# Kernel tuning notes

Measured on AMD Instinct MI355X. Metric: run time of the kernel, lower is better.

Reference implementation:

```python
import jax, jax.numpy as jnp
import numpy as np

N = 100000   # nodes
E = 1600000  # edges
D_IN, D_H, D_OUT = 128, 128, 64
BN_EPS = 1e-5


def setup_inputs() -> dict:
    key = jax.random.key(0)
    ks = jax.random.split(key, 12)

    def lin_w(k, fan_in, shape):
        s = 1.0 / np.sqrt(fan_in)
        return jax.random.uniform(k, shape, jnp.float32, -s, s)

    return {
        "x": jax.random.normal(ks[0], (N, D_IN), jnp.float32),
        "edge_index": jax.random.randint(ks[1], (2, E), 0, N, dtype=jnp.int64),
        "edge_weight": jax.random.uniform(ks[2], (E,), jnp.float32),
        "W1": lin_w(ks[3], D_IN, (D_IN, D_H)),
        "b1": jnp.zeros((D_H,), jnp.float32),
        "W2": lin_w(ks[4], D_H, (D_H, D_H)),
        "b2": jnp.zeros((D_H,), jnp.float32),
        "W3": lin_w(ks[5], D_H, (D_H, D_OUT)),
        "b3": jnp.zeros((D_OUT,), jnp.float32),
        "gamma1": jnp.ones((D_H,), jnp.float32),
        "beta1": jnp.zeros((D_H,), jnp.float32),
        "gamma2": jnp.ones((D_H,), jnp.float32),
        "beta2": jnp.zeros((D_H,), jnp.float32),
    }


def _gcn_conv(x, src, dst, w, W, b):
    # PyG GCNConv: x' = D^{-1/2} (A + I) D^{-1/2} (x W) + b, self-loop weight 1
    n = x.shape[0]
    h = x @ W                                   # [N, d_out]
    loop = jnp.arange(n, dtype=src.dtype)
    s = jnp.concatenate([src, loop])            # [E+N]
    d = jnp.concatenate([dst, loop])
    ww = jnp.concatenate([w, jnp.ones((n,), w.dtype)])
    deg = jax.ops.segment_sum(ww, d, num_segments=n)          # in-degree at targets
    dinv = jnp.where(deg > 0, jax.lax.rsqrt(deg), 0.0)
    norm = dinv[s] * ww * dinv[d]               # [E+N]
    msg = h[s] * norm[:, None]                  # gather + scale
    out = jax.ops.segment_sum(msg, d, num_segments=n)
    return out + b


def _batch_norm(x, gamma, beta):
    mean = jnp.mean(x, axis=0)
    var = jnp.mean(jnp.square(x - mean), axis=0)  # biased, as BatchNorm uses
    return (x - mean) * jax.lax.rsqrt(var + BN_EPS) * gamma + beta


def reference(x, edge_index, edge_weight, W1, b1, W2, b2, W3, b3,
              gamma1, beta1, gamma2, beta2):
    src, dst = edge_index[0], edge_index[1]
    h = _gcn_conv(x, src, dst, edge_weight, W1, b1)
    h = jax.nn.relu(_batch_norm(h, gamma1, beta1))
    h = _gcn_conv(h, src, dst, edge_weight, W2, b2)
    h = jax.nn.relu(_batch_norm(h, gamma2, beta2))
    return _gcn_conv(h, src, dst, edge_weight, W3, b3)
```

## Files before the change

### kernel.cpp

```cpp
#include <hip/hip_runtime.h>
#include <hip/hip_fp16.h>
#include <cstdint>
#include <cstddef>

#define BN_EPS 1e-5f
#define FPSCALE 268435456.0f

typedef _Float16 half8 __attribute__((ext_vector_type(8)));
typedef float floatx4 __attribute__((ext_vector_type(4)));

__device__ __forceinline__ float loadS(const __half* p) { return __half2float(*p); }
__device__ __forceinline__ float2 load2(const __half* p) {
    return __half22float2(*(const __half2*)p);
}
__device__ __forceinline__ void storeS(float* p, float v) { *p = v; }
__device__ __forceinline__ void storeS(__half* p, float v) { *p = __float2half(v); }
__device__ __forceinline__ void store2(float* p, float a, float b) {
    *(float2*)p = make_float2(a, b);
}
__device__ __forceinline__ void store2(__half* p, float a, float b) {
    *(__half2*)p = __floats2half2_rn(a, b);
}
__device__ __forceinline__ float wn_of(unsigned v) {
    __half_raw hr; hr.x = (unsigned short)(v & 0x7fffu);
    return __half2float((__half)hr);
}

__global__ void detect_mode_kernel(const unsigned* __restrict__ p, int nwords, int* mode) {
    __shared__ unsigned red[256];
    unsigned m = 0;
    for (int i = 1 + 2 * (int)threadIdx.x; i < nwords; i += 512) m |= p[i];
    red[threadIdx.x] = m;
    __syncthreads();
    for (int s = 128; s > 0; s >>= 1) {
        if ((int)threadIdx.x < s) red[threadIdx.x] |= red[threadIdx.x + s];
        __syncthreads();
    }
    if (threadIdx.x == 0) mode[0] = (red[0] == 0) ? 1 : 0;
}

static __device__ __forceinline__ int load_edge(const void* ei, int mode64, long long pos) {
    if (mode64) return (int)((const long long*)ei)[pos];
    return ((const int*)ei)[pos];
}

__global__ void fill_packed_kernel(unsigned long long* __restrict__ packed, int N) {
    int i = blockIdx.x * 256 + threadIdx.x;
    if (i < N) packed[i] = 0ULL;
}

__global__ void histogram_kernel(const void* __restrict__ ei, const float* __restrict__ ew,
                                 unsigned long long* __restrict__ packed,
                                 unsigned* __restrict__ rank,
                                 const int* __restrict__ mode, int E) {
    int e = blockIdx.x * 256 + threadIdx.x;
    if (e >= E) return;
    int md = *mode;
    int d = load_edge(ei, md, (long long)E + e);
    unsigned long long contrib = (1ULL << 40) | (unsigned long long)(ew[e] * FPSCALE);
    unsigned long long old = atomicAdd(&packed[d], contrib);
    rank[e] = (unsigned)(old >> 40);
}

__global__ void unpack_kernel(const unsigned long long* __restrict__ packed,
                              float* __restrict__ dinv, int* __restrict__ cnt, int N) {
    int i = blockIdx.x * 256 + threadIdx.x;
    if (i < N) {
        unsigned long long p = packed[i];
        cnt[i] = (int)(p >> 40);
        float deg = 1.0f + (float)(p & 0xFFFFFFFFFFULL) * (1.0f / FPSCALE);
        dinv[i] = rsqrtf(deg);
    }
}

__global__ void scan_phaseA_kernel(const int* __restrict__ cnt, int* __restrict__ bsum, int N) {
    __shared__ int red[256];
    int base = blockIdx.x * 2048 + (int)threadIdx.x * 8;
    int s = 0;
#pragma unroll
    for (int j = 0; j < 8; ++j) { int idx = base + j; if (idx < N) s += cnt[idx]; }
    red[threadIdx.x] = s;
    __syncthreads();
    for (int st = 128; st > 0; st >>= 1) {
        if ((int)threadIdx.x < st) red[threadIdx.x] += red[threadIdx.x + st];
        __syncthreads();
    }
    if (threadIdx.x == 0) bsum[blockIdx.x] = red[0];
}

__global__ void scan_phaseB_kernel(int* __restrict__ bsum, int G) {
    if (threadIdx.x == 0 && blockIdx.x == 0) {
        int run = 0;
        for (int i = 0; i < G; ++i) { int t = bsum[i]; bsum[i] = run; run += t; }
    }
}

__global__ void scan_phaseC_kernel(const int* __restrict__ cnt, const int* __restrict__ bsum,
                                   int* __restrict__ row_start, int N) {
    __shared__ int lds[256];
    int tid = threadIdx.x;
    int base = blockIdx.x * 2048 + tid * 8;
    int vals[8];
    int s = 0;
#pragma unroll
    for (int j = 0; j < 8; ++j) {
        int idx = base + j;
        int v = (idx < N) ? cnt[idx] : 0;
        vals[j] = s;
        s += v;
    }
    lds[tid] = s;
    __syncthreads();
    for (int off = 1; off < 256; off <<= 1) {
        int t = 0;
        if (tid >= off) t = lds[tid - off];
        __syncthreads();
        lds[tid] += t;
        __syncthreads();
    }
    int excl = lds[tid] - s;
    int b = bsum[blockIdx.x] + excl;
#pragma unroll
    for (int j = 0; j < 8; ++j) {
        int idx = base + j;
        if (idx < N) row_start[idx] = b + vals[j];
    }
}

__global__ void scatter_kernel(const void* __restrict__ ei, const float* __restrict__ ew,
                               const float* __restrict__ dinv,
                               const int* __restrict__ row_start,
                               const unsigned* __restrict__ rank,
                               unsigned* __restrict__ edata,
                               const int* __restrict__ mode, int E) {
    int e = blockIdx.x * 256 + threadIdx.x;
    if (e >= E) return;
    int md = *mode;
    int s = load_edge(ei, md, e);
    int d = load_edge(ei, md, (long long)E + e);
    float wn = dinv[s] * ew[e] * dinv[d];
    unsigned hb = (unsigned)__half_as_ushort(__float2half(wn)) & 0x7fffu;
    edata[row_start[d] + (int)rank[e]] = ((unsigned)s << 15) | hb;
}

template <int M>
__global__ void transpose_w_kernel(const float* __restrict__ W, _Float16* __restrict__ WT) {
    int t = blockIdx.x * 256 + (int)threadIdx.x;
    if (t < 128 * M) {
        int n = t / 128, k = t % 128;
        WT[t] = (_Float16)W[k * M + n];
    }
}

template <int M, bool BN, typename TI>
__global__ __launch_bounds__(256) void gemm_mfma_kernel(const TI* __restrict__ X,
                                                        const _Float16* __restrict__ WTg,
                                                        const float* __restrict__ sc,
                                                        const float* __restrict__ sh,
                                                        __half* __restrict__ Hout, int N) {
    constexpr int CT = M / 16;
    constexpr int LDK = 128 + 8;
    __shared__ _Float16 WT[M * LDK];

    for (int t = threadIdx.x; t < M * 16; t += 256) {
        int n = t / 16, seg = t % 16;
        *(half8*)&WT[n * LDK + seg * 8] = *(const half8*)&WTg[n * 128 + seg * 8];
    }
    __syncthreads();

    const int wave = (int)threadIdx.x >> 6;
    const int lane = (int)threadIdx.x & 63;
    const int qd = lane >> 4;
    const int ln = lane & 15;
    const int tile0 = blockIdx.x * 64 + wave * 16;
    int ar = tile0 + ln;
    if (ar >= N) ar = N - 1;

    half8 aF[4];
    const TI* xr = X + (size_t)ar * 128 + qd * 8;
#pragma unroll
    for (int kb = 0; kb < 4; ++kb) {
        float vv[8];
        if constexpr (sizeof(TI) == 4) {
            float4 v0 = *(const float4*)(xr + kb * 32);
            float4 v1 = *(const float4*)(xr + kb * 32 + 4);
            vv[0] = v0.x; vv[1] = v0.y; vv[2] = v0.z; vv[3] = v0.w;
            vv[4] = v1.x; vv[5] = v1.y; vv[6] = v1.z; vv[7] = v1.w;
        } else {
            half8 raw = *(const half8*)(xr + kb * 32);
#pragma unroll
            for (int j = 0; j < 8; ++j) vv[j] = (float)raw[j];
        }
        if (BN) {
            const int kbase = kb * 32 + qd * 8;
#pragma unroll
            for (int j = 0; j < 8; ++j)
                vv[j] = fmaxf(fmaf(vv[j], sc[kbase + j], sh[kbase + j]), 0.0f);
        }
        half8 a;
#pragma unroll
        for (int j = 0; j < 8; ++j) a[j] = (_Float16)vv[j];
        aF[kb] = a;
    }

#pragma unroll
    for (int ct = 0; ct < CT; ++ct) {
        floatx4 acc = {0.0f, 0.0f, 0.0f, 0.0f};
#pragma unroll
        for (int kb = 0; kb < 4; ++kb) {
            half8 b = *(const half8*)&WT[(ct * 16 + ln) * LDK + kb * 32 + qd * 8];
            acc = __builtin_amdgcn_mfma_f32_16x16x32_f16(aF[kb], b, acc, 0, 0, 0);
        }
#pragma unroll
        for (int r = 0; r < 4; ++r) {
            int orow = tile0 + qd * 4 + r;
            if (orow < N) Hout[(size_t)orow * M + ct * 16 + ln] = __float2half(acc[r]);
        }
    }
}

template <int D, bool BIAS, typename TY>
__global__ __launch_bounds__(64) void agg_kernel(const __half* __restrict__ H,
                                                 const unsigned* __restrict__ edata,
                                                 const int* __restrict__ row_start,
                                                 const int* __restrict__ cnt,
                                                 const float* __restrict__ dinv,
                                                 const float* __restrict__ bias,
                                                 TY* __restrict__ Y, int N) {
    constexpr int VPT = D / 64;
    __shared__ unsigned eb[64];
    const int i = blockIdx.x;
    const int t = (int)threadIdx.x;
    const int c0 = t * VPT;
    const float di = dinv[i];
    const float dii = di * di;

    float acc0, acc1 = 0.0f;
    if constexpr (VPT == 2) {
        float2 h = load2(H + (size_t)i * D + c0);
        acc0 = dii * h.x;
        acc1 = dii * h.y;
    } else {
        acc0 = dii * loadS(H + (size_t)i * D + c0);
    }

    const int base = row_start[i];
    const int n = cnt[i];
    for (int off = 0; off < n; off += 64) {
        const int m = min(64, n - off);
        if (t < m) eb[t] = edata[base + off + t];
        __syncthreads();
        int j = 0;
        for (; j + 4 <= m; j += 4) {
            const unsigned e0 = eb[j], e1 = eb[j + 1], e2 = eb[j + 2], e3 = eb[j + 3];
            const float w0 = wn_of(e0), w1 = wn_of(e1), w2 = wn_of(e2), w3 = wn_of(e3);
            if constexpr (VPT == 2) {
                float2 h0 = load2(H + (size_t)(e0 >> 15) * D + c0);
                float2 h1 = load2(H + (size_t)(e1 >> 15) * D + c0);
                float2 h2 = load2(H + (size_t)(e2 >> 15) * D + c0);
                float2 h3 = load2(H + (size_t)(e3 >> 15) * D + c0);
                acc0 = fmaf(w0, h0.x, acc0); acc1 = fmaf(w0, h0.y, acc1);
                acc0 = fmaf(w1, h1.x, acc0); acc1 = fmaf(w1, h1.y, acc1);
                acc0 = fmaf(w2, h2.x, acc0); acc1 = fmaf(w2, h2.y, acc1);
                acc0 = fmaf(w3, h3.x, acc0); acc1 = fmaf(w3, h3.y, acc1);
            } else {
                float h0 = loadS(H + (size_t)(e0 >> 15) * D + c0);
                float h1 = loadS(H + (size_t)(e1 >> 15) * D + c0);
                float h2 = loadS(H + (size_t)(e2 >> 15) * D + c0);
                float h3 = loadS(H + (size_t)(e3 >> 15) * D + c0);
                acc0 = fmaf(w0, h0, acc0);
                acc0 = fmaf(w1, h1, acc0);
                acc0 = fmaf(w2, h2, acc0);
                acc0 = fmaf(w3, h3, acc0);
            }
        }
        for (; j < m; ++j) {
            const unsigned e = eb[j];
            const float wn = wn_of(e);
            const size_t rb = (size_t)(e >> 15) * D + c0;
            if constexpr (VPT == 2) {
                float2 h = load2(H + rb);
                acc0 = fmaf(wn, h.x, acc0);
                acc1 = fmaf(wn, h.y, acc1);
            } else {
                acc0 = fmaf(wn, loadS(H + rb), acc0);
            }
        }
        __syncthreads();
    }

    if constexpr (VPT == 2) {
        if (BIAS) { acc0 += bias[c0]; acc1 += bias[c0 + 1]; }
        store2(Y + (size_t)i * D + c0, acc0, acc1);
    } else {
        if (BIAS) acc0 += bias[c0];
        storeS(Y + (size_t)i * D + c0, acc0);
    }
}

__global__ void zero_stats_kernel(float* __restrict__ gsum, float* __restrict__ gsq) {
    int t = threadIdx.x;
    if (t < 128) { gsum[t] = 0.0f; gsq[t] = 0.0f; }
}

__global__ void stats_kernel(const __half* __restrict__ Y, float* __restrict__ gsum,
                             float* __restrict__ gsq, int N) {
    __shared__ float ls[256], lq[256];
    const int tid = threadIdx.x;
    const int c = tid & 127;
    const int half_ = tid >> 7;
    float s = 0.0f, q = 0.0f;
    for (int row = blockIdx.x * 2 + half_; row < N; row += 512) {
        float v = __half2float(Y[(size_t)row * 128 + c]);
        s += v;
        q = fmaf(v, v, q);
    }
    ls[tid] = s; lq[tid] = q;
    __syncthreads();
    if (tid < 128) {
        atomicAdd(&gsum[c], ls[tid] + ls[tid + 128]);
        atomicAdd(&gsq[c],  lq[tid] + lq[tid + 128]);
    }
}

__global__ void finalize_stats_kernel(const float* __restrict__ gsum, const float* __restrict__ gsq,
                                      const float* __restrict__ gamma, const float* __restrict__ beta,
                                      float* __restrict__ sc, float* __restrict__ sh, int N) {
    int t = threadIdx.x;
    if (t < 128) {
        float inv_n = 1.0f / (float)N;
        float mean = gsum[t] * inv_n;
        float var = gsq[t] * inv_n - mean * mean;
        float scale = gamma[t] * rsqrtf(var + BN_EPS);
        sc[t] = scale;
        sh[t] = beta[t] - mean * scale;
    }
}

extern "C" void kernel_launch(void* const* d_in, const int* in_sizes, int n_in,
                              void* d_out, int out_size, void* d_ws, size_t ws_size,
                              hipStream_t stream) {
    const float* x   = (const float*)d_in[0];
    const void*  ei  = d_in[1];
    const float* ew  = (const float*)d_in[2];
    const float* W1  = (const float*)d_in[3];
    const float* W2  = (const float*)d_in[5];
    const float* W3  = (const float*)d_in[7];
    const float* b3  = (const float*)d_in[8];
    const float* g1  = (const float*)d_in[9];
    const float* be1 = (const float*)d_in[10];
    const float* g2  = (const float*)d_in[11];
    const float* be2 = (const float*)d_in[12];
    float* out = (float*)d_out;

    const int N = in_sizes[0] / 128;
    const int E = in_sizes[2];
    const int G = (N + 2047) / 2048;

    char* w = (char*)d_ws;
    size_t off = 0;
    auto alloc = [&](size_t bytes) -> void* {
        void* p = w + off;
        off += (bytes + 255) & ~(size_t)255;
        return p;
    };
    unsigned long long* packed = (unsigned long long*)alloc((size_t)N * 8);
    float* dinv      = (float*)alloc((size_t)N * 4);
    int*   cnt       = (int*)  alloc((size_t)N * 4);
    int*   row_start = (int*)  alloc((size_t)N * 4);
    unsigned* rank   = (unsigned*)alloc((size_t)E * 4);
    unsigned* edata  = (unsigned*)alloc((size_t)E * 4);
    int*   bsum      = (int*)  alloc((size_t)G * 4);
    int*   mode      = (int*)  alloc(256);
    float* gsum      = (float*)alloc(128 * 4);
    float* gsq       = (float*)alloc(128 * 4);
    float* scb       = (float*)alloc(128 * 4);
    float* shb       = (float*)alloc(128 * 4);
    _Float16* WT1    = (_Float16*)alloc(128 * 128 * 2);
    _Float16* WT2    = (_Float16*)alloc(128 * 128 * 2);
    _Float16* WT3    = (_Float16*)alloc(128 * 64 * 2);
    __half* H        = (__half*)alloc((size_t)N * 128 * 2);
    __half* Yh       = (__half*)alloc((size_t)N * 128 * 2);
    (void)ws_size; (void)n_in; (void)out_size;

    const int nb = (N + 255) / 256;
    const int ebk = (E + 255) / 256;
    const int gb = (N + 63) / 64;

    detect_mode_kernel<<<1, 256, 0, stream>>>((const unsigned*)ei, 4096, mode);
    fill_packed_kernel<<<nb, 256, 0, stream>>>(packed, N);
    histogram_kernel<<<ebk, 256, 0, stream>>>(ei, ew, packed, rank, mode, E);
    unpack_kernel<<<nb, 256, 0, stream>>>(packed, dinv, cnt, N);
    scan_phaseA_kernel<<<G, 256, 0, stream>>>(cnt, bsum, N);
    scan_phaseB_kernel<<<1, 1, 0, stream>>>(bsum, G);
    scan_phaseC_kernel<<<G, 256, 0, stream>>>(cnt, bsum, row_start, N);
    scatter_kernel<<<ebk, 256, 0, stream>>>(ei, ew, dinv, row_start, rank, edata, mode, E);

    transpose_w_kernel<128><<<64, 256, 0, stream>>>(W1, WT1);
    transpose_w_kernel<128><<<64, 256, 0, stream>>>(W2, WT2);
    transpose_w_kernel<64><<<32, 256, 0, stream>>>(W3, WT3);

    gemm_mfma_kernel<128, false, float><<<gb, 256, 0, stream>>>(x, WT1, nullptr, nullptr, H, N);
    agg_kernel<128, false, __half><<<N, 64, 0, stream>>>(H, edata, row_start, cnt, dinv, nullptr, Yh, N);
    zero_stats_kernel<<<1, 128, 0, stream>>>(gsum, gsq);
    stats_kernel<<<256, 256, 0, stream>>>(Yh, gsum, gsq, N);
    finalize_stats_kernel<<<1, 128, 0, stream>>>(gsum, gsq, g1, be1, scb, shb, N);

    gemm_mfma_kernel<128, true, __half><<<gb, 256, 0, stream>>>(Yh, WT2, scb, shb, H, N);
    agg_kernel<128, false, __half><<<N, 64, 0, stream>>>(H, edata, row_start, cnt, dinv, nullptr, Yh, N);
    zero_stats_kernel<<<1, 128, 0, stream>>>(gsum, gsq);
    stats_kernel<<<256, 256, 0, stream>>>(Yh, gsum, gsq, N);
    finalize_stats_kernel<<<1, 128, 0, stream>>>(gsum, gsq, g2, be2, scb, shb, N);

    gemm_mfma_kernel<64, true, __half><<<gb, 256, 0, stream>>>(Yh, WT3, scb, shb, H, N);
    agg_kernel<64, true, float><<<N, 64, 0, stream>>>(H, edata, row_start, cnt, dinv, b3, out, N);
}
```

Before: 562.6 us.

## Merge setup kernels and run graph aggregation with shuffle broadcast, four nodes per block

Combines many small launches into fewer kernels. Mode detection, packed zeroing and weight transposes now share one init kernel. The histogram runs alongside the first GEMM. Unpack is merged with scan phase A, and the serial phase B is replaced by a per-block prefix sum in scan C. Stats zeroing is folded into the scatter and GEMM kernels. The aggregation kernel now handles four nodes per 256-thread block, one wave per node. It broadcasts edge data with wave shuffles instead of LDS and __syncthreads, and unrolls the gather loop by eight, relying on padded zero-weight entries for the tail. The aim is to cut launch overhead and barrier cost, in exchange for a little redundant bsum summation and extra gathers of row 0 on the tail.

```diff
diff --git a/kernel.cpp b/kernel.cpp
--- a/kernel.cpp
+++ b/kernel.cpp
@@ -26,141 +26,65 @@
     return __half2float((__half)hr);
 }
 
-__global__ void detect_mode_kernel(const unsigned* __restrict__ p, int nwords, int* mode) {
-    __shared__ unsigned red[256];
-    unsigned m = 0;
-    for (int i = 1 + 2 * (int)threadIdx.x; i < nwords; i += 512) m |= p[i];
-    red[threadIdx.x] = m;
-    __syncthreads();
-    for (int s = 128; s > 0; s >>= 1) {
-        if ((int)threadIdx.x < s) red[threadIdx.x] |= red[threadIdx.x + s];
-        __syncthreads();
-    }
-    if (threadIdx.x == 0) mode[0] = (red[0] == 0) ? 1 : 0;
-}
-
 static __device__ __forceinline__ int load_edge(const void* ei, int mode64, long long pos) {
     if (mode64) return (int)((const long long*)ei)[pos];
     return ((const int*)ei)[pos];
 }
 
-__global__ void fill_packed_kernel(unsigned long long* __restrict__ packed, int N) {
-    int i = blockIdx.x * 256 + threadIdx.x;
-    if (i < N) packed[i] = 0ULL;
-}
-
-__global__ void histogram_kernel(const void* __restrict__ ei, const float* __restrict__ ew,
-                                 unsigned long long* __restrict__ packed,
-                                 unsigned* __restrict__ rank,
-                                 const int* __restrict__ mode, int E) {
-    int e = blockIdx.x * 256 + threadIdx.x;
-    if (e >= E) return;
-    int md = *mode;
-    int d = load_edge(ei, md, (long long)E + e);
-    unsigned long long contrib = (1ULL << 40) | (unsigned long long)(ew[e] * FPSCALE);
-    unsigned long long old = atomicAdd(&packed[d], contrib);
-    rank[e] = (unsigned)(old >> 40);
-}
-
-__global__ void unpack_kernel(const unsigned long long* __restrict__ packed,
-                              float* __restrict__ dinv, int* __restrict__ cnt, int N) {
-    int i = blockIdx.x * 256 + threadIdx.x;
-    if (i < N) {
-        unsigned long long p = packed[i];
-        cnt[i] = (int)(p >> 40);
-        float deg = 1.0f + (float)(p & 0xFFFFFFFFFFULL) * (1.0f / FPSCALE);
-        dinv[i] = rsqrtf(deg);
-    }
-}
-
-__global__ void scan_phaseA_kernel(const int* __restrict__ cnt, int* __restrict__ bsum, int N) {
-    __shared__ int red[256];
-    int base = blockIdx.x * 2048 + (int)threadIdx.x * 8;
-    int s = 0;
-#pragma unroll
-    for (int j = 0; j < 8; ++j) { int idx = base + j; if (idx < N) s += cnt[idx]; }
-    red[threadIdx.x] = s;
-    __syncthreads();
-    for (int st = 128; st > 0; st >>= 1) {
-        if ((int)threadIdx.x < st) red[threadIdx.x] += red[threadIdx.x + st];
+__global__ __launch_bounds__(256) void init_kernel(const unsigned* __restrict__ eiw, int nwords,
+                                                   int* __restrict__ mode,
+                                                   unsigned long long* __restrict__ packed, int N,
+                                                   const float* __restrict__ W1,
+                                                   const float* __restrict__ W2,
+                                                   const float* __restrict__ W3,
+                                                   _Float16* __restrict__ WT1,
+                                                   _Float16* __restrict__ WT2,
+                                                   _Float16* __restrict__ WT3, int nb) {
+    __shared__ unsigned red[256];
+    const int bid = (int)blockIdx.x;
+    const int tid = (int)threadIdx.x;
+    if (bid < nb) {
+        int i = bid * 256 + tid;
+        if (i < N) packed[i] = 0ULL;
+        return;
+    }
+    if (bid == nb) {
+        unsigned m = 0;
+        for (int i = 1 + 2 * tid; i < nwords; i += 512) m |= eiw[i];
+        red[tid] = m;
         __syncthreads();
-    }
-    if (threadIdx.x == 0) bsum[blockIdx.x] = red[0];
-}
-
-__global__ void scan_phaseB_kernel(int* __restrict__ bsum, int G) {
-    if (threadIdx.x == 0 && blockIdx.x == 0) {
-        int run = 0;
-        for (int i = 0; i < G; ++i) { int t = bsum[i]; bsum[i] = run; run += t; }
-    }
-}
-
-__global__ void scan_phaseC_kernel(const int* __restrict__ cnt, const int* __restrict__ bsum,
-                                   int* __restrict__ row_start, int N) {
-    __shared__ int lds[256];
-    int tid = threadIdx.x;
-    int base = blockIdx.x * 2048 + tid * 8;
-    int vals[8];
-    int s = 0;
-#pragma unroll
-    for (int j = 0; j < 8; ++j) {
-        int idx = base + j;
-        int v = (idx < N) ? cnt[idx] : 0;
-        vals[j] = s;
-        s += v;
-    }
-    lds[tid] = s;
-    __syncthreads();
-    for (int off = 1; off < 256; off <<= 1) {
-        int t = 0;
-        if (tid >= off) t = lds[tid - off];
-        __syncthreads();
-        lds[tid] += t;
-        __syncthreads();
-    }
-    int excl = lds[tid] - s;
-    int b = bsum[blockIdx.x] + excl;
-#pragma unroll
-    for (int j = 0; j < 8; ++j) {
-        int idx = base + j;
-        if (idx < N) row_start[idx] = b + vals[j];
-    }
-}
-
-__global__ void scatter_kernel(const void* __restrict__ ei, const float* __restrict__ ew,
-                               const float* __restrict__ dinv,
-                               const int* __restrict__ row_start,
-                               const unsigned* __restrict__ rank,
-                               unsigned* __restrict__ edata,
-                               const int* __restrict__ mode, int E) {
-    int e = blockIdx.x * 256 + threadIdx.x;
-    if (e >= E) return;
-    int md = *mode;
-    int s = load_edge(ei, md, e);
-    int d = load_edge(ei, md, (long long)E + e);
-    float wn = dinv[s] * ew[e] * dinv[d];
-    unsigned hb = (unsigned)__half_as_ushort(__float2half(wn)) & 0x7fffu;
-    edata[row_start[d] + (int)rank[e]] = ((unsigned)s << 15) | hb;
-}
-
-template <int M>
-__global__ void transpose_w_kernel(const float* __restrict__ W, _Float16* __restrict__ WT) {
-    int t = blockIdx.x * 256 + (int)threadIdx.x;
-    if (t < 128 * M) {
+        for (int s = 128; s > 0; s >>= 1) {
+            if (tid < s) red[tid] |= red[tid + s];
+            __syncthreads();
+        }
+        if (tid == 0) mode[0] = (red[0] == 0) ? 1 : 0;
+        return;
+    }
+    const int t_ = bid - nb - 1;
+    if (t_ < 64) {
+        int t = t_ * 256 + tid;
         int n = t / 128, k = t % 128;
-        WT[t] = (_Float16)W[k * M + n];
+        WT1[t] = (_Float16)W1[k * 128 + n];
+    } else if (t_ < 128) {
+        int t = (t_ - 64) * 256 + tid;
+        int n = t / 128, k = t % 128;
+        WT2[t] = (_Float16)W2[k * 128 + n];
+    } else {
+        int t = (t_ - 128) * 256 + tid;
+        int n = t / 128, k = t % 128;
+        WT3[t] = (_Float16)W3[k * 64 + n];
     }
 }
 
 template <int M, bool BN, typename TI>
-__global__ __launch_bounds__(256) void gemm_mfma_kernel(const TI* __restrict__ X,
-                                                        const _Float16* __restrict__ WTg,
-                                                        const float* __restrict__ sc,
-                                                        const float* __restrict__ sh,
-                                                        __half* __restrict__ Hout, int N) {
+__device__ __forceinline__ void gemm_body(int gbid, const TI* __restrict__ X,
+                                          const _Float16* __restrict__ WTg,
+                                          const float* __restrict__ sc,
+                                          const float* __restrict__ sh,
+                                          __half* __restrict__ Hout, int N,
+                                          _Float16* WT ) {
     constexpr int CT = M / 16;
-    constexpr int LDK = 128 + 8;
-    __shared__ _Float16 WT[M * LDK];
+    constexpr int LDK = 136;
 
     for (int t = threadIdx.x; t < M * 16; t += 256) {
         int n = t / 16, seg = t % 16;
@@ -172,7 +96,7 @@
     const int lane = (int)threadIdx.x & 63;
     const int qd = lane >> 4;
     const int ln = lane & 15;
-    const int tile0 = blockIdx.x * 64 + wave * 16;
+    const int tile0 = gbid * 64 + wave * 16;
     int ar = tile0 + ln;
     if (ar >= N) ar = N - 1;
 
@@ -219,19 +143,127 @@
     }
 }
 
+__global__ __launch_bounds__(256) void hist_gemm1_kernel(const void* __restrict__ ei,
+                                                         const float* __restrict__ ew,
+                                                         unsigned long long* __restrict__ packed,
+                                                         unsigned* __restrict__ rank,
+                                                         const int* __restrict__ mode, int E, int GB,
+                                                         const float* __restrict__ X,
+                                                         const _Float16* __restrict__ WT1g,
+                                                         __half* __restrict__ Hout, int N) {
+    __shared__ _Float16 WT[128 * 136];
+    if ((int)blockIdx.x < GB) {
+        gemm_body<128, false, float>(blockIdx.x, X, WT1g, nullptr, nullptr, Hout, N, WT);
+        return;
+    }
+    int e = ((int)blockIdx.x - GB) * 256 + (int)threadIdx.x;
+    if (e >= E) return;
+    int md = *mode;
+    int d = load_edge(ei, md, (long long)E + e);
+    unsigned long long contrib = (1ULL << 40) | (unsigned long long)(ew[e] * FPSCALE);
+    unsigned long long old = atomicAdd(&packed[d], contrib);
+    rank[e] = (unsigned)(old >> 40);
+}
+
+__global__ __launch_bounds__(256) void unpack_scanA_kernel(const unsigned long long* __restrict__ packed,
+                                                           float* __restrict__ dinv,
+                                                           int* __restrict__ cnt,
+                                                           int* __restrict__ bsum, int N) {
+    __shared__ int red[256];
+    const int tid = (int)threadIdx.x;
+    const int base = (int)blockIdx.x * 2048 + tid * 8;
+    int s = 0;
+#pragma unroll
+    for (int j = 0; j < 8; ++j) {
+        int idx = base + j;
+        if (idx < N) {
+            unsigned long long p = packed[idx];
+            int c = (int)(p >> 40);
+            cnt[idx] = c;
+            dinv[idx] = rsqrtf(1.0f + (float)(p & 0xFFFFFFFFFFULL) * (1.0f / FPSCALE));
+            s += c;
+        }
+    }
+    red[tid] = s;
+    __syncthreads();
+    for (int st = 128; st > 0; st >>= 1) {
+        if (tid < st) red[tid] += red[tid + st];
+        __syncthreads();
+    }
+    if (tid == 0) bsum[blockIdx.x] = red[0];
+}
+
+__global__ __launch_bounds__(256) void scanC_kernel(const int* __restrict__ cnt,
+                                                    const int* __restrict__ bsum,
+                                                    int* __restrict__ row_start, int N) {
+    __shared__ int lds[256];
+    const int tid = (int)threadIdx.x;
+    int gbase = 0;
+    for (int j = 0; j < (int)blockIdx.x; ++j) gbase += bsum[j];
+    const int base = (int)blockIdx.x * 2048 + tid * 8;
+    int vals[8];
+    int s = 0;
+#pragma unroll
+    for (int j = 0; j < 8; ++j) {
+        int idx = base + j;
+        int v = (idx < N) ? cnt[idx] : 0;
+        vals[j] = s;
+        s += v;
+    }
+    lds[tid] = s;
+    __syncthreads();
+    for (int off = 1; off < 256; off <<= 1) {
+        int t = 0;
+        if (tid >= off) t = lds[tid - off];
+        __syncthreads();
+        lds[tid] += t;
+        __syncthreads();
+    }
+    int excl = lds[tid] - s;
+    int b = gbase + excl;
+#pragma unroll
+    for (int j = 0; j < 8; ++j) {
+        int idx = base + j;
+        if (idx < N) row_start[idx] = b + vals[j];
+    }
+}
+
+__global__ __launch_bounds__(256) void scatter_zero_kernel(const void* __restrict__ ei,
+                                                           const float* __restrict__ ew,
+                                                           const float* __restrict__ dinv,
+                                                           const int* __restrict__ row_start,
+                                                           const unsigned* __restrict__ rank,
+                                                           unsigned* __restrict__ edata,
+                                                           const int* __restrict__ mode, int E, int EBK,
+                                                           float* __restrict__ gsum,
+                                                           float* __restrict__ gsq) {
+    if ((int)blockIdx.x == EBK) {
+        if (threadIdx.x < 128) { gsum[threadIdx.x] = 0.0f; gsq[threadIdx.x] = 0.0f; }
+        return;
+    }
+    int e = (int)blockIdx.x * 256 + (int)threadIdx.x;
+    if (e >= E) return;
+    int md = *mode;
+    int s = load_edge(ei, md, e);
+    int d = load_edge(ei, md, (long long)E + e);
+    float wn = dinv[s] * ew[e] * dinv[d];
+    unsigned hb = (unsigned)__half_as_ushort(__float2half(wn)) & 0x7fffu;
+    edata[row_start[d] + (int)rank[e]] = ((unsigned)s << 15) | hb;
+}
+
 template <int D, bool BIAS, typename TY>
-__global__ __launch_bounds__(64) void agg_kernel(const __half* __restrict__ H,
-                                                 const unsigned* __restrict__ edata,
-                                                 const int* __restrict__ row_start,
-                                                 const int* __restrict__ cnt,
-                                                 const float* __restrict__ dinv,
-                                                 const float* __restrict__ bias,
-                                                 TY* __restrict__ Y, int N) {
+__global__ __launch_bounds__(256) void agg_kernel(const __half* __restrict__ H,
+                                                  const unsigned* __restrict__ edata,
+                                                  const int* __restrict__ row_start,
+                                                  const int* __restrict__ cnt,
+                                                  const float* __restrict__ dinv,
+                                                  const float* __restrict__ bias,
+                                                  TY* __restrict__ Y, int N) {
     constexpr int VPT = D / 64;
-    __shared__ unsigned eb[64];
-    const int i = blockIdx.x;
-    const int t = (int)threadIdx.x;
-    const int c0 = t * VPT;
+    const int lane = (int)threadIdx.x & 63;
+    const int i = (int)blockIdx.x * 4 + ((int)threadIdx.x >> 6);
+    if (i >= N) return;
+    const int c0 = lane * VPT;
     const float di = dinv[i];
     const float dii = di * di;
 
@@ -247,46 +279,51 @@
     const int base = row_start[i];
     const int n = cnt[i];
     for (int off = 0; off < n; off += 64) {
-        const int m = min(64, n - off);
-        if (t < m) eb[t] = edata[base + off + t];
-        __syncthreads();
-        int j = 0;
-        for (; j + 4 <= m; j += 4) {
-            const unsigned e0 = eb[j], e1 = eb[j + 1], e2 = eb[j + 2], e3 = eb[j + 3];
-            const float w0 = wn_of(e0), w1 = wn_of(e1), w2 = wn_of(e2), w3 = wn_of(e3);
+        const int rem = n - off;
+        unsigned ev = 0;
+        if (lane < rem) ev = edata[base + off + lane];
+        const int mm = min(64, rem);
+        for (int j = 0; j < mm; j += 8) {
+            const unsigned e0 = __shfl(ev, j),     e1 = __shfl(ev, j + 1);
+            const unsigned e2 = __shfl(ev, j + 2), e3 = __shfl(ev, j + 3);
+            const unsigned e4 = __shfl(ev, j + 4), e5 = __shfl(ev, j + 5);
+            const unsigned e6 = __shfl(ev, j + 6), e7 = __shfl(ev, j + 7);
             if constexpr (VPT == 2) {
                 float2 h0 = load2(H + (size_t)(e0 >> 15) * D + c0);
                 float2 h1 = load2(H + (size_t)(e1 >> 15) * D + c0);
                 float2 h2 = load2(H + (size_t)(e2 >> 15) * D + c0);
                 float2 h3 = load2(H + (size_t)(e3 >> 15) * D + c0);
-                acc0 = fmaf(w0, h0.x, acc0); acc1 = fmaf(w0, h0.y, acc1);
-                acc0 = fmaf(w1, h1.x, acc0); acc1 = fmaf(w1, h1.y, acc1);
-                acc0 = fmaf(w2, h2.x, acc0); acc1 = fmaf(w2, h2.y, acc1);
-                acc0 = fmaf(w3, h3.x, acc0); acc1 = fmaf(w3, h3.y, acc1);
+                float2 h4 = load2(H + (size_t)(e4 >> 15) * D + c0);
+                float2 h5 = load2(H + (size_t)(e5 >> 15) * D + c0);
+                float2 h6 = load2(H + (size_t)(e6 >> 15) * D + c0);
+                float2 h7 = load2(H + (size_t)(e7 >> 15) * D + c0);
+                acc0 = fmaf(wn_of(e0), h0.x, acc0); acc1 = fmaf(wn_of(e0), h0.y, acc1);
+                acc0 = fmaf(wn_of(e1), h1.x, acc0); acc1 = fmaf(wn_of(e1), h1.y, acc1);
+                acc0 = fmaf(wn_of(e2), h2.x, acc0); acc1 = fmaf(wn_of(e2), h2.y, acc1);
+                acc0 = fmaf(wn_of(e3), h3.x, acc0); acc1 = fmaf(wn_of(e3), h3.y, acc1);
+                acc0 = fmaf(wn_of(e4), h4.x, acc0); acc1 = fmaf(wn_of(e4), h4.y, acc1);
+                acc0 = fmaf(wn_of(e5), h5.x, acc0); acc1 = fmaf(wn_of(e5), h5.y, acc1);
+                acc0 = fmaf(wn_of(e6), h6.x, acc0); acc1 = fmaf(wn_of(e6), h6.y, acc1);
+                acc0 = fmaf(wn_of(e7), h7.x, acc0); acc1 = fmaf(wn_of(e7), h7.y, acc1);
             } else {
                 float h0 = loadS(H + (size_t)(e0 >> 15) * D + c0);
                 float h1 = loadS(H + (size_t)(e1 >> 15) * D + c0);
                 float h2 = loadS(H + (size_t)(e2 >> 15) * D + c0);
                 float h3 = loadS(H + (size_t)(e3 >> 15) * D + c0);
-                acc0 = fmaf(w0, h0, acc0);
-                acc0 = fmaf(w1, h1, acc0);
-                acc0 = fmaf(w2, h2, acc0);
-                acc0 = fmaf(w3, h3, acc0);
+                float h4 = loadS(H + (size_t)(e4 >> 15) * D + c0);
+                float h5 = loadS(H + (size_t)(e5 >> 15) * D + c0);
+                float h6 = loadS(H + (size_t)(e6 >> 15) * D + c0);
+                float h7 = loadS(H + (size_t)(e7 >> 15) * D + c0);
+                acc0 = fmaf(wn_of(e0), h0, acc0);
+                acc0 = fmaf(wn_of(e1), h1, acc0);
+                acc0 = fmaf(wn_of(e2), h2, acc0);
+                acc0 = fmaf(wn_of(e3), h3, acc0);
+                acc0 = fmaf(wn_of(e4), h4, acc0);
+                acc0 = fmaf(wn_of(e5), h5, acc0);
+                acc0 = fmaf(wn_of(e6), h6, acc0);
+                acc0 = fmaf(wn_of(e7), h7, acc0);
             }
         }
-        for (; j < m; ++j) {
-            const unsigned e = eb[j];
-            const float wn = wn_of(e);
-            const size_t rb = (size_t)(e >> 15) * D + c0;
-            if constexpr (VPT == 2) {
-                float2 h = load2(H + rb);
-                acc0 = fmaf(wn, h.x, acc0);
-                acc1 = fmaf(wn, h.y, acc1);
-            } else {
-                acc0 = fmaf(wn, loadS(H + rb), acc0);
-            }
-        }
-        __syncthreads();
     }
 
     if constexpr (VPT == 2) {
@@ -298,9 +335,20 @@
     }
 }
 
-__global__ void zero_stats_kernel(float* __restrict__ gsum, float* __restrict__ gsq) {
-    int t = threadIdx.x;
-    if (t < 128) { gsum[t] = 0.0f; gsq[t] = 0.0f; }
+template <int M, bool BN, typename TI, bool ZERO>
+__global__ __launch_bounds__(256) void gemm_mfma_kernel(const TI* __restrict__ X,
+                                                        const _Float16* __restrict__ WTg,
+                                                        const float* __restrict__ sc,
+                                                        const float* __restrict__ sh,
+                                                        __half* __restrict__ Hout, int N,
+                                                        float* __restrict__ gsum,
+                                                        float* __restrict__ gsq, int GB) {
+    __shared__ _Float16 WT[M * 136];
+    if (ZERO && (int)blockIdx.x == GB) {
+        if (threadIdx.x < 128) { gsum[threadIdx.x] = 0.0f; gsq[threadIdx.x] = 0.0f; }
+        return;
+    }
+    gemm_body<M, BN, TI>(blockIdx.x, X, WTg, sc, sh, Hout, N, WT);
 }
 
 __global__ void stats_kernel(const __half* __restrict__ Y, float* __restrict__ gsum,
@@ -383,35 +431,29 @@
     __half* Yh       = (__half*)alloc((size_t)N * 128 * 2);
     (void)ws_size; (void)n_in; (void)out_size;
 
-    const int nb = (N + 255) / 256;
+    const int nb  = (N + 255) / 256;
     const int ebk = (E + 255) / 256;
-    const int gb = (N + 63) / 64;
-
-    detect_mode_kernel<<<1, 256, 0, stream>>>((const unsigned*)ei, 4096, mode);
-    fill_packed_kernel<<<nb, 256, 0, stream>>>(packed, N);
-    histogram_kernel<<<ebk, 256, 0, stream>>>(ei, ew, packed, rank, mode, E);
-    unpack_kernel<<<nb, 256, 0, stream>>>(packed, dinv, cnt, N);
-    scan_phaseA_kernel<<<G, 256, 0, stream>>>(cnt, bsum, N);
-    scan_phaseB_kernel<<<1, 1, 0, stream>>>(bsum, G);
-    scan_phaseC_kernel<<<G, 256, 0, stream>>>(cnt, bsum, row_start, N);
-    scatter_kernel<<<ebk, 256, 0, stream>>>(ei, ew, dinv, row_start, rank, edata, mode, E);
-
-    transpose_w_kernel<128><<<64, 256, 0, stream>>>(W1, WT1);
-    transpose_w_kernel<128><<<64, 256, 0, stream>>>(W2, WT2);
-    transpose_w_kernel<64><<<32, 256, 0, stream>>>(W3, WT3);
-
-    gemm_mfma_kernel<128, false, float><<<gb, 256, 0, stream>>>(x, WT1, nullptr, nullptr, H, N);
-    agg_kernel<128, false, __half><<<N, 64, 0, stream>>>(H, edata, row_start, cnt, dinv, nullptr, Yh, N);
-    zero_stats_kernel<<<1, 128, 0, stream>>>(gsum, gsq);
+    const int gb  = (N + 63) / 64;
+    const int ab  = (N + 3) / 4;
+
+    init_kernel<<<nb + 1 + 160, 256, 0, stream>>>((const unsigned*)ei, 4096, mode, packed, N,
+                                                  W1, W2, W3, WT1, WT2, WT3, nb);
+    hist_gemm1_kernel<<<gb + ebk, 256, 0, stream>>>(ei, ew, packed, rank, mode, E, gb,
+                                                    x, WT1, H, N);
+    unpack_scanA_kernel<<<G, 256, 0, stream>>>(packed, dinv, cnt, bsum, N);
+    scanC_kernel<<<G, 256, 0, stream>>>(cnt, bsum, row_start, N);
+    scatter_zero_kernel<<<ebk + 1, 256, 0, stream>>>(ei, ew, dinv, row_start, rank, edata,
+                                                     mode, E, ebk, gsum, gsq);
+
+    agg_kernel<128, false, __half><<<ab, 256, 0, stream>>>(H, edata, row_start, cnt, dinv, nullptr, Yh, N);
     stats_kernel<<<256, 256, 0, stream>>>(Yh, gsum, gsq, N);
     finalize_stats_kernel<<<1, 128, 0, stream>>>(gsum, gsq, g1, be1, scb, shb, N);
 
-    gemm_mfma_kernel<128, true, __half><<<gb, 256, 0, stream>>>(Yh, WT2, scb, shb, H, N);
-    agg_kernel<128, false, __half><<<N, 64, 0, stream>>>(H, edata, row_start, cnt, dinv, nullptr, Yh, N);
-    zero_stats_kernel<<<1, 128, 0, stream>>>(gsum, gsq);
+    gemm_mfma_kernel<128, true, __half, true><<<gb + 1, 256, 0, stream>>>(Yh, WT2, scb, shb, H, N, gsum, gsq, gb);
+    agg_kernel<128, false, __half><<<ab, 256, 0, stream>>>(H, edata, row_start, cnt, dinv, nullptr, Yh, N);
     stats_kernel<<<256, 256, 0, stream>>>(Yh, gsum, gsq, N);
     finalize_stats_kernel<<<1, 128, 0, stream>>>(gsum, gsq, g2, be2, scb, shb, N);
 
-    gemm_mfma_kernel<64, true, __half><<<gb, 256, 0, stream>>>(Yh, WT3, scb, shb, H, N);
-    agg_kernel<64, true, float><<<N, 64, 0, stream>>>(H, edata, row_start, cnt, dinv, b3, out, N);
-}
+    gemm_mfma_kernel<64, true, __half, false><<<gb, 256, 0, stream>>>(Yh, WT3, scb, shb, H, N, nullptr, nullptr, gb);
+    agg_kernel<64, true, float><<<ab, 256, 0, stream>>>(H, edata, row_start, cnt, dinv, b3, out, N);
+}
```

Result: faster. 543.3 us (-3.4%).
